# Kernel optimization log

Measured on AMD Instinct MI355X. Metric: run time of the kernel, lower is better.

## Reference

```python
import jax, jax.numpy as jnp
import numpy as np

B, N, INDIM = 512, 200, 200
D1, D2, D3 = 32, 32, 8
RATIO = 0.5
K1 = int(np.ceil(RATIO * N))    # 100 nodes kept after pool1
K2 = int(np.ceil(RATIO * K1))   # 50 nodes kept after pool2
BN_EPS = 1e-5
NEG = -1e9


def setup_inputs() -> dict:
    key = jax.random.key(0)
    ks = jax.random.split(key, 16)
    x = jax.random.normal(ks[0], (B, N, INDIM), jnp.float32)
    u = jax.random.uniform(ks[1], (B, N, N), jnp.float32)
    ut = jnp.triu(jnp.where(u > 0.9, u, 0.0), 1)
    adj = ut + jnp.swapaxes(ut, 1, 2)
    g = lambda i, shape: jax.random.normal(ks[i], shape, jnp.float32) * 0.1
    return dict(
        x=x, adj=adj,
        W1=g(2, (INDIM, D1)), a1s=g(3, (D1,)), a1d=g(4, (D1,)), b1=jnp.zeros((D1,), jnp.float32),
        W2=g(5, (D1, D2)), a2s=g(6, (D2,)), a2d=g(7, (D2,)), b2=jnp.zeros((D2,), jnp.float32),
        pw1=g(8, (D1,)), pw2=g(9, (D2,)),
        fc1_w=g(10, ((D1 + D2) * 2, D2)), fc1_b=jnp.zeros((D2,), jnp.float32),
        fc2_w=g(11, (D2, D3)), fc2_b=jnp.zeros((D3,), jnp.float32),
        fc3_w=g(12, (D3, 2)), fc3_b=jnp.zeros((2,), jnp.float32),
        bn4_g=jnp.ones((D2,), jnp.float32), bn4_b=jnp.zeros((D2,), jnp.float32),
        bn5_g=jnp.ones((D3,), jnp.float32), bn5_b=jnp.zeros((D3,), jnp.float32))


def _gat(x, mask, W, a_s, a_d, b):
    # PyG GATConv (heads=1): alpha_ij = softmax_j LeakyReLU(a_d.h_i + a_s.h_j) over in-neighbors j (self-loops added)
    h = jnp.einsum('bnf,fd->bnd', x, W)
    es = h @ a_s                    # [B,n] source term
    ed = h @ a_d                    # [B,n] dest term
    m = mask | jnp.eye(mask.shape[1], dtype=bool)
    logits = jax.nn.leaky_relu(ed[:, :, None] + es[:, None, :], 0.2)
    alpha = jax.nn.softmax(jnp.where(m, logits, NEG), axis=-1)   # [B,n,n]
    return jnp.einsum('bij,bjd->bid', alpha, h) + b


def _topk(x, adj_w, w, k):
    # TopKPooling(multiplier=1, nonlinearity=sigmoid): score = sigmoid(x.w/||w||)
    score = jax.nn.sigmoid((x @ w) / (jnp.linalg.norm(w) + 1e-16))   # [B,n]
    vals, idx = jax.lax.top_k(score, k)                              # perm sorted desc, as PyG
    xk = jnp.take_along_axis(x, idx[:, :, None], axis=1) * vals[:, :, None]
    ak = jnp.take_along_axis(jnp.take_along_axis(adj_w, idx[:, :, None], axis=1), idx[:, None, :], axis=2)
    return xk, ak, vals


def _bn(z, g, b):
    # eval-mode BatchNorm1d: running_mean=0, running_var=1
    return g * z / jnp.sqrt(1.0 + BN_EPS) + b


def reference(x, adj, W1, a1s, a1d, b1, W2, a2s, a2d, b2, pw1, pw2,
              fc1_w, fc1_b, fc2_w, fc2_b, fc3_w, fc3_b, bn4_g, bn4_b, bn5_g, bn5_b):
    h = _gat(x, adj > 0, W1, a1s, a1d, b1)
    h, aw, s1 = _topk(h, adj, pw1, K1)
    x1 = jnp.concatenate([h.max(axis=1), h.mean(axis=1)], axis=1)    # [B, 64]
    # augment_adj: add self-loops, spspmm (A+I)@(A+I), remove self-loops
    eye = jnp.eye(K1, dtype=aw.dtype)
    a2 = jnp.einsum('bij,bjk->bik', aw + eye, aw + eye) * (1.0 - eye)
    h = _gat(h, a2 != 0, W2, a2s, a2d, b2)
    h, _, s2 = _topk(h, a2, pw2, K2)
    x2 = jnp.concatenate([h.max(axis=1), h.mean(axis=1)], axis=1)    # [B, 64]
    z = jnp.concatenate([x1, x2], axis=1)                            # [B, 128]
    z = _bn(jax.nn.relu(z @ fc1_w + fc1_b), bn4_g, bn4_b)            # dropout: eval -> identity
    z = _bn(jax.nn.relu(z @ fc2_w + fc2_b), bn5_g, bn5_b)
    logp = jax.nn.log_softmax(z @ fc3_w + fc3_b, axis=-1)            # [B, 2]
    return logp, s1, s2
```

## Files before the change

### kernel.cpp

```cpp
#include <hip/hip_runtime.h>
#include <math.h>

#define N_   200
#define B_   512
#define K1_  100
#define K2_  50

#define S1_OFF 1024
#define S2_OFF 52224

__device__ __forceinline__ float lrelu(float v) { return v > 0.f ? v : 0.2f * v; }
__device__ __forceinline__ float sigm(float v)  { return 1.f / (1.f + __expf(-v)); }

__device__ __forceinline__ void bitonic_desc(float* key, int* idx, int n, int t) {
  for (int k = 2; k <= n; k <<= 1) {
    for (int j = k >> 1; j > 0; j >>= 1) {
      __syncthreads();
      int ixj = t ^ j;
      if (t < n && ixj > t) {
        float a = key[t], c = key[ixj];
        int ia = idx[t], ic = idx[ixj];
        bool gt = (a > c) || (a == c && ia < ic);
        if (((t & k) == 0) ? !gt : gt) {
          key[t] = c; key[ixj] = a; idx[t] = ic; idx[ixj] = ia;
        }
      }
    }
  }
  __syncthreads();
}


__global__ __launch_bounds__(256) void gnn_fused(
    const float* __restrict__ x, const float* __restrict__ adj,
    const float* __restrict__ W1, const float* __restrict__ a1s,
    const float* __restrict__ a1d, const float* __restrict__ b1,
    const float* __restrict__ W2g, const float* __restrict__ a2s,
    const float* __restrict__ a2d, const float* __restrict__ b2,
    const float* __restrict__ pw1, const float* __restrict__ pw2,
    const float* __restrict__ fc1w, const float* __restrict__ fc1b,
    const float* __restrict__ fc2w, const float* __restrict__ fc2b,
    const float* __restrict__ fc3w, const float* __restrict__ fc3b,
    const float* __restrict__ bn4g, const float* __restrict__ bn4b,
    const float* __restrict__ bn5g, const float* __restrict__ bn5b,
    float* __restrict__ out)
{
  __shared__ __align__(16) char smem[63792];
  float*    sH    = (float*)smem;
  float*    sH1   = (float*)(smem + 25600);
  float*    sXK   = (float*)(smem + 38400);
  float*    sES   = (float*)(smem + 51200);
  float*    sED   = (float*)(smem + 52000);
  unsigned* sBITS = (unsigned*)(smem + 52800);
  float*    sW2   = (float*)(smem + 52800);
  float*    sKey  = (float*)(smem + 58400);
  int*      sIdx  = (int*)(smem + 59424);
  int*      sSel  = (int*)(smem + 60448);
  float*    sVal  = (float*)(smem + 60848);
  float*    sXV   = (float*)(smem + 61248);
  float*    sRed  = (float*)(smem + 61760);
  unsigned* sMask2= (unsigned*)(smem + 61792);

  const int t = threadIdx.x;
  const int b = blockIdx.x;
  const float* xb = x   + (size_t)b * N_ * N_;
  const float* ab = adj + (size_t)b * N_ * N_;

  if (t < N_) {
    float acc[32];
    #pragma unroll
    for (int d = 0; d < 32; ++d) acc[d] = 0.f;
    const float* xr = xb + t * N_;
    for (int k = 0; k < N_; k += 4) {
      float4 xv = *(const float4*)(xr + k);
      #pragma unroll
      for (int kk = 0; kk < 4; ++kk) {
        float xs = (&xv.x)[kk];
        const float* wr = W1 + (k + kk) * 32;
        #pragma unroll
        for (int d = 0; d < 32; ++d) acc[d] += xs * wr[d];
      }
    }
    float es = 0.f, ed = 0.f;
    #pragma unroll
    for (int d = 0; d < 32; ++d) { es += acc[d] * a1s[d]; ed += acc[d] * a1d[d]; }
    sES[t] = es; sED[t] = ed;
    #pragma unroll
    for (int d = 0; d < 32; ++d) sH[t * 32 + d] = acc[d];
  }
  __syncthreads();

  {
    float v = (t < N_) ? sES[t] : -3.0e38f;
    #pragma unroll
    for (int off = 1; off < 64; off <<= 1) v = fmaxf(v, __shfl_xor(v, off, 64));
    if ((t & 63) == 0) sRed[t >> 6] = v;
  }
  __syncthreads();
  {
    float esmax = fmaxf(fmaxf(sRed[0], sRed[1]), fmaxf(sRed[2], sRed[3]));

    if (t < N_) {
      const float* arow = ab + (size_t)t * N_;
      float ed_i = sED[t];
      float L = lrelu(ed_i + esmax);
      float ssum = 0.f;
      float acc[32];
      #pragma unroll
      for (int d = 0; d < 32; ++d) acc[d] = 0.f;
      for (int jw = 0; jw < 7; ++jw) {
        int jbase = jw * 32;
        int cnt = (jw < 6) ? 32 : 8;
        unsigned mb = 0u;
        for (int j4 = 0; j4 < cnt; j4 += 4) {
          float4 av = *(const float4*)(arow + jbase + j4);
          #pragma unroll
          for (int jj = 0; jj < 4; ++jj) {
            int j = jbase + j4 + jj;
            float a = (&av.x)[jj];
            bool conn = a > 0.f;
            if (conn) mb |= (1u << (j4 + jj));
            float w = 0.f;
            if (conn || j == t) w = __expf(lrelu(ed_i + sES[j]) - L);
            ssum += w;
            const float* hr = &sH[j * 32];
            #pragma unroll
            for (int d = 0; d < 32; ++d) acc[d] += w * hr[d];
          }
        }
        sBITS[t * 7 + jw] = mb;
      }
      float inv = 1.f / ssum;
      #pragma unroll
      for (int d = 0; d < 32; ++d) sH1[t * 32 + d] = acc[d] * inv + b1[d];
    }
  }
  __syncthreads();

  {
    float npw = 0.f;
    #pragma unroll
    for (int d = 0; d < 32; ++d) npw += pw1[d] * pw1[d];
    npw = sqrtf(npw) + 1e-16f;
    float sc = -1.f;
    if (t < N_) {
      float dp = 0.f;
      #pragma unroll
      for (int d = 0; d < 32; ++d) dp += sH1[t * 32 + d] * pw1[d];
      sc = sigm(dp / npw);
    }
    sKey[t] = sc; sIdx[t] = t;
  }
  bitonic_desc(sKey, sIdx, 256, t);
  if (t < K1_) {
    out[S1_OFF + b * K1_ + t] = sKey[t];
    sVal[t] = sKey[t]; sSel[t] = sIdx[t];
  }
  __syncthreads();
  {
    float tmp[13];
    #pragma unroll
    for (int it = 0; it < 13; ++it) {
      int i = t + it * 256;
      if (i < K1_ * 32) tmp[it] = sH1[sSel[i >> 5] * 32 + (i & 31)] * sVal[i >> 5];
    }
    __syncthreads();
    #pragma unroll
    for (int it = 0; it < 13; ++it) {
      int i = t + it * 256;
      if (i < K1_ * 32) sXK[i] = tmp[it];
    }
  }
  __syncthreads();
  if (t < 32) {
    float m = -3.0e38f, s = 0.f;
    for (int r = 0; r < K1_; ++r) { float v = sXK[r * 32 + t]; m = fmaxf(m, v); s += v; }
    sXV[t] = m; sXV[32 + t] = s / 100.f;
  }

  if (t < K1_) {
    int gi = sSel[t];
    #pragma unroll
    for (int w = 0; w < 4; ++w) {
      unsigned m = 0;
      const int lim = (w < 3) ? 32 : 4;
      for (int jj = 0; jj < lim; ++jj) {
        int j = w * 32 + jj;
        int gj = sSel[j];
        unsigned bit = (sBITS[gi * 7 + (gj >> 5)] >> (gj & 31)) & 1u;
        if (j == t) bit = 1u;
        m |= bit << jj;
      }
      sMask2[t * 5 + w] = m;
    }
  }
  __syncthreads();
  {
    unsigned pr0 = 0, pr1 = 0, pr2 = 0, pr3 = 0;
    if (t < K1_) {
      #pragma unroll
      for (int kw = 0; kw < 4; ++kw) {
        unsigned mk = sMask2[t * 5 + kw];
        const int lim = (kw < 3) ? 32 : 4;
        for (int kk = 0; kk < lim; ++kk) {
          if ((mk >> kk) & 1u) {
            int k = kw * 32 + kk;
            pr0 |= sMask2[k * 5 + 0]; pr1 |= sMask2[k * 5 + 1];
            pr2 |= sMask2[k * 5 + 2]; pr3 |= sMask2[k * 5 + 3];
          }
        }
      }
    }
    __syncthreads();
    if (t < K1_) {
      sMask2[t * 5 + 0] = pr0; sMask2[t * 5 + 1] = pr1;
      sMask2[t * 5 + 2] = pr2; sMask2[t * 5 + 3] = pr3;
    }
  }
  __syncthreads();

  for (int i = t; i < 1024; i += 256) sW2[i] = W2g[i];
  __syncthreads();
  if (t < K1_) {
    float acc[32];
    #pragma unroll
    for (int d = 0; d < 32; ++d) acc[d] = 0.f;
    for (int k = 0; k < 32; ++k) {
      float xv = sXK[t * 32 + k];
      const float* wr = &sW2[k * 32];
      #pragma unroll
      for (int d = 0; d < 32; ++d) acc[d] += xv * wr[d];
    }
    float es = 0.f, ed = 0.f;
    #pragma unroll
    for (int d = 0; d < 32; ++d) { es += acc[d] * a2s[d]; ed += acc[d] * a2d[d]; }
    sES[t] = es; sED[t] = ed;
    #pragma unroll
    for (int d = 0; d < 32; ++d) sH[t * 32 + d] = acc[d];
  }
  __syncthreads();
  {
    float v = (t < K1_) ? sES[t] : -3.0e38f;
    #pragma unroll
    for (int off = 1; off < 64; off <<= 1) v = fmaxf(v, __shfl_xor(v, off, 64));
    if ((t & 63) == 0) sRed[t >> 6] = v;
  }
  __syncthreads();
  {
    float esm2 = fmaxf(fmaxf(sRed[0], sRed[1]), fmaxf(sRed[2], sRed[3]));
    if (t < K1_) {
      float ed_i = sED[t];
      float L = lrelu(ed_i + esm2);
      float ssum = 0.f;
      float acc[32];
      #pragma unroll
      for (int d = 0; d < 32; ++d) acc[d] = 0.f;
      #pragma unroll
      for (int jw = 0; jw < 4; ++jw) {
        unsigned mw = sMask2[t * 5 + jw];
        const int lim = (jw < 3) ? 32 : 4;
        for (int jj = 0; jj < lim; ++jj) {
          int j = jw * 32 + jj;
          float w = 0.f;
          if ((mw >> jj) & 1u) w = __expf(lrelu(ed_i + sES[j]) - L);
          ssum += w;
          const float* hr = &sH[j * 32];
          #pragma unroll
          for (int d = 0; d < 32; ++d) acc[d] += w * hr[d];
        }
      }
      float inv = 1.f / ssum;
      #pragma unroll
      for (int d = 0; d < 32; ++d) sH1[t * 32 + d] = acc[d] * inv + b2[d];
    }
  }
  __syncthreads();

  {
    float npw = 0.f;
    #pragma unroll
    for (int d = 0; d < 32; ++d) npw += pw2[d] * pw2[d];
    npw = sqrtf(npw) + 1e-16f;
    float sc = -1.f;
    if (t < K1_) {
      float dp = 0.f;
      #pragma unroll
      for (int d = 0; d < 32; ++d) dp += sH1[t * 32 + d] * pw2[d];
      sc = sigm(dp / npw);
    }
    if (t < 128) { sKey[t] = sc; sIdx[t] = t; }
  }
  bitonic_desc(sKey, sIdx, 128, t);
  if (t < K2_) {
    out[S2_OFF + b * K2_ + t] = sKey[t];
    sVal[t] = sKey[t]; sSel[t] = sIdx[t];
  }
  __syncthreads();
  {
    int d = t & 31, r0 = t >> 5;
    for (int r = r0; r < K2_; r += 8) sXK[r * 32 + d] = sH1[sSel[r] * 32 + d] * sVal[r];
  }
  __syncthreads();
  if (t < 32) {
    float m = -3.0e38f, s = 0.f;
    for (int r = 0; r < K2_; ++r) { float v = sXK[r * 32 + t]; m = fmaxf(m, v); s += v; }
    sXV[64 + t] = m; sXV[96 + t] = s / 50.f;
  }
  __syncthreads();

  const float RS = 0.99999500003749969f;
  if (t < 32) {
    float z = fc1b[t];
    for (int k = 0; k < 128; ++k) z += sXV[k] * fc1w[k * 32 + t];
    z = fmaxf(z, 0.f);
    z = bn4g[t] * z * RS + bn4b[t];
    sKey[t] = z;
  }
  __syncthreads();
  if (t < 8) {
    float z = fc2b[t];
    for (int k = 0; k < 32; ++k) z += sKey[k] * fc2w[k * 8 + t];
    z = fmaxf(z, 0.f);
    z = bn5g[t] * z * RS + bn5b[t];
    sKey[32 + t] = z;
  }
  __syncthreads();
  if (t < 2) {
    float z = fc3b[t];
    for (int k = 0; k < 8; ++k) z += sKey[32 + k] * fc3w[k * 2 + t];
    sKey[40 + t] = z;
  }
  __syncthreads();
  if (t < 2) {
    float z0 = sKey[40], z1 = sKey[41];
    float m = fmaxf(z0, z1);
    float lse = m + logf(__expf(z0 - m) + __expf(z1 - m));
    out[b * 2 + t] = sKey[40 + t] - lse;
  }
}

extern "C" void kernel_launch(void* const* d_in, const int* in_sizes, int n_in,
                              void* d_out, int out_size, void* d_ws, size_t ws_size,
                              hipStream_t stream) {
  (void)in_sizes; (void)n_in; (void)d_ws; (void)ws_size; (void)out_size;
  const float* x    = (const float*)d_in[0];
  const float* adj  = (const float*)d_in[1];
  const float* W1   = (const float*)d_in[2];
  const float* a1s  = (const float*)d_in[3];
  const float* a1d  = (const float*)d_in[4];
  const float* b1   = (const float*)d_in[5];
  const float* W2   = (const float*)d_in[6];
  const float* a2s  = (const float*)d_in[7];
  const float* a2d  = (const float*)d_in[8];
  const float* b2   = (const float*)d_in[9];
  const float* pw1  = (const float*)d_in[10];
  const float* pw2  = (const float*)d_in[11];
  const float* fc1w = (const float*)d_in[12];
  const float* fc1b = (const float*)d_in[13];
  const float* fc2w = (const float*)d_in[14];
  const float* fc2b = (const float*)d_in[15];
  const float* fc3w = (const float*)d_in[16];
  const float* fc3b = (const float*)d_in[17];
  const float* bn4g = (const float*)d_in[18];
  const float* bn4b = (const float*)d_in[19];
  const float* bn5g = (const float*)d_in[20];
  const float* bn5b = (const float*)d_in[21];

  gnn_fused<<<B_, 256, 0, stream>>>(x, adj, W1, a1s, a1d, b1, W2, a2s, a2d, b2,
                                    pw1, pw2, fc1w, fc1b, fc2w, fc2b, fc3w, fc3b,
                                    bn4g, bn4b, bn5g, bn5b, (float*)d_out);
}
```

Baseline: 332.6 us.

## Split feature dimension across 512 threads per block with padded shared rows

Doubles the block to 512 threads and splits the 32-wide feature dimension across thread groups: 2 groups of 16 for GAT1 and 4 groups of 8 for GAT2. Partial attention scalars are reduced through extra shared buffers. Shared rows are padded to a stride of 36 to reduce bank conflicts, and the W2 load is moved earlier to overlap with mask squaring. The aim is more parallelism per graph and lower per-thread register use, at the cost of more shared memory (lower blocks per CU) and duplicated adjacency reads and exp work across the feature groups.

```diff
diff --git a/kernel.cpp b/kernel.cpp
--- a/kernel.cpp
+++ b/kernel.cpp
@@ -5,6 +5,7 @@
 #define B_   512
 #define K1_  100
 #define K2_  50
+#define ST   36
 
 #define S1_OFF 1024
 #define S2_OFF 52224
@@ -31,7 +32,7 @@
 }
 
 
-__global__ __launch_bounds__(256) void gnn_fused(
+__global__ __launch_bounds__(512, 4) void gnn_fused(
     const float* __restrict__ x, const float* __restrict__ adj,
     const float* __restrict__ W1, const float* __restrict__ a1s,
     const float* __restrict__ a1d, const float* __restrict__ b1,
@@ -45,95 +46,109 @@
     const float* __restrict__ bn5g, const float* __restrict__ bn5b,
     float* __restrict__ out)
 {
-  __shared__ __align__(16) char smem[63792];
+  __shared__ __align__(16) char smem[74736];
   float*    sH    = (float*)smem;
-  float*    sH1   = (float*)(smem + 25600);
-  float*    sXK   = (float*)(smem + 38400);
-  float*    sES   = (float*)(smem + 51200);
-  float*    sED   = (float*)(smem + 52000);
-  unsigned* sBITS = (unsigned*)(smem + 52800);
-  float*    sW2   = (float*)(smem + 52800);
-  float*    sKey  = (float*)(smem + 58400);
-  int*      sIdx  = (int*)(smem + 59424);
-  int*      sSel  = (int*)(smem + 60448);
-  float*    sVal  = (float*)(smem + 60848);
-  float*    sXV   = (float*)(smem + 61248);
-  float*    sRed  = (float*)(smem + 61760);
-  unsigned* sMask2= (unsigned*)(smem + 61792);
+  float*    sH1   = (float*)(smem + 28800);
+  float*    sXK   = (float*)(smem + 43200);
+  float*    sES   = (float*)(smem + 57600);
+  float*    sED   = (float*)(smem + 58624);
+  float*    sES2  = (float*)(smem + 59648);
+  float*    sED2  = (float*)(smem + 61696);
+  unsigned* sBITS = (unsigned*)(smem + 63744);
+  float*    sW2   = (float*)(smem + 63744);
+  float*    sKey  = (float*)(smem + 69344);
+  int*      sIdx  = (int*)(smem + 70368);
+  int*      sSel  = (int*)(smem + 71392);
+  float*    sVal  = (float*)(smem + 71792);
+  float*    sXV   = (float*)(smem + 72192);
+  float*    sRed  = (float*)(smem + 72704);
+  unsigned* sMask2= (unsigned*)(smem + 72736);
 
   const int t = threadIdx.x;
   const int b = blockIdx.x;
+  const int n = t & 255;
+  const int d0 = __builtin_amdgcn_readfirstlane((t >> 8) << 4);
   const float* xb = x   + (size_t)b * N_ * N_;
   const float* ab = adj + (size_t)b * N_ * N_;
 
-  if (t < N_) {
-    float acc[32];
-    #pragma unroll
-    for (int d = 0; d < 32; ++d) acc[d] = 0.f;
-    const float* xr = xb + t * N_;
+  if (n < N_) {
+    float acc[16];
+    #pragma unroll
+    for (int d = 0; d < 16; ++d) acc[d] = 0.f;
+    const float* xr = xb + n * N_;
+    const float* Wh = W1 + d0;
     for (int k = 0; k < N_; k += 4) {
       float4 xv = *(const float4*)(xr + k);
       #pragma unroll
       for (int kk = 0; kk < 4; ++kk) {
         float xs = (&xv.x)[kk];
-        const float* wr = W1 + (k + kk) * 32;
+        const float* wr = Wh + (k + kk) * 32;
         #pragma unroll
-        for (int d = 0; d < 32; ++d) acc[d] += xs * wr[d];
+        for (int d = 0; d < 16; ++d) acc[d] += xs * wr[d];
       }
     }
     float es = 0.f, ed = 0.f;
     #pragma unroll
-    for (int d = 0; d < 32; ++d) { es += acc[d] * a1s[d]; ed += acc[d] * a1d[d]; }
-    sES[t] = es; sED[t] = ed;
-    #pragma unroll
-    for (int d = 0; d < 32; ++d) sH[t * 32 + d] = acc[d];
-  }
-  __syncthreads();
-
-  {
-    float v = (t < N_) ? sES[t] : -3.0e38f;
+    for (int d = 0; d < 16; ++d) { es += acc[d] * a1s[d0 + d]; ed += acc[d] * a1d[d0 + d]; }
+    sES2[t] = es; sED2[t] = ed;
+    #pragma unroll
+    for (int d = 0; d < 16; ++d) sH[n * ST + d0 + d] = acc[d];
+  }
+  __syncthreads();
+
+  float esmax;
+  {
+    float v = -3.0e38f;
+    if (t < N_) {
+      float es = sES2[t] + sES2[t + 256];
+      float ed = sED2[t] + sED2[t + 256];
+      sES[t] = es; sED[t] = ed; v = es;
+    }
     #pragma unroll
     for (int off = 1; off < 64; off <<= 1) v = fmaxf(v, __shfl_xor(v, off, 64));
     if ((t & 63) == 0) sRed[t >> 6] = v;
   }
   __syncthreads();
   {
-    float esmax = fmaxf(fmaxf(sRed[0], sRed[1]), fmaxf(sRed[2], sRed[3]));
-
-    if (t < N_) {
-      const float* arow = ab + (size_t)t * N_;
-      float ed_i = sED[t];
-      float L = lrelu(ed_i + esmax);
-      float ssum = 0.f;
-      float acc[32];
-      #pragma unroll
-      for (int d = 0; d < 32; ++d) acc[d] = 0.f;
-      for (int jw = 0; jw < 7; ++jw) {
-        int jbase = jw * 32;
-        int cnt = (jw < 6) ? 32 : 8;
-        unsigned mb = 0u;
-        for (int j4 = 0; j4 < cnt; j4 += 4) {
-          float4 av = *(const float4*)(arow + jbase + j4);
+    float m = sRed[0];
+    #pragma unroll
+    for (int i = 1; i < 8; ++i) m = fmaxf(m, sRed[i]);
+    esmax = m;
+  }
+
+  if (n < N_) {
+    const float* arow = ab + (size_t)n * N_;
+    float ed_i = sED[n];
+    float L = lrelu(ed_i + esmax);
+    float ssum = 0.f;
+    float acc[16];
+    #pragma unroll
+    for (int d = 0; d < 16; ++d) acc[d] = 0.f;
+    for (int jw = 0; jw < 7; ++jw) {
+      int jbase = jw * 32;
+      int cnt = (jw < 6) ? 32 : 8;
+      unsigned mb = 0u;
+      for (int j4 = 0; j4 < cnt; j4 += 4) {
+        float4 av = *(const float4*)(arow + jbase + j4);
+        #pragma unroll
+        for (int jj = 0; jj < 4; ++jj) {
+          int j = jbase + j4 + jj;
+          float a = (&av.x)[jj];
+          bool conn = a > 0.f;
+          if (conn) mb |= (1u << (j4 + jj));
+          float w = 0.f;
+          if (conn || j == n) w = __expf(lrelu(ed_i + sES[j]) - L);
+          ssum += w;
+          const float* hr = &sH[j * ST + d0];
           #pragma unroll
-          for (int jj = 0; jj < 4; ++jj) {
-            int j = jbase + j4 + jj;
-            float a = (&av.x)[jj];
-            bool conn = a > 0.f;
-            if (conn) mb |= (1u << (j4 + jj));
-            float w = 0.f;
-            if (conn || j == t) w = __expf(lrelu(ed_i + sES[j]) - L);
-            ssum += w;
-            const float* hr = &sH[j * 32];
-            #pragma unroll
-            for (int d = 0; d < 32; ++d) acc[d] += w * hr[d];
-          }
+          for (int d = 0; d < 16; ++d) acc[d] += w * hr[d];
         }
-        sBITS[t * 7 + jw] = mb;
-      }
-      float inv = 1.f / ssum;
-      #pragma unroll
-      for (int d = 0; d < 32; ++d) sH1[t * 32 + d] = acc[d] * inv + b1[d];
-    }
+      }
+      if (d0 == 0) sBITS[n * 7 + jw] = mb;
+    }
+    float inv = 1.f / ssum;
+    #pragma unroll
+    for (int d = 0; d < 16; ++d) sH1[n * ST + d0 + d] = acc[d] * inv + b1[d0 + d];
   }
   __syncthreads();
 
@@ -146,10 +161,10 @@
     if (t < N_) {
       float dp = 0.f;
       #pragma unroll
-      for (int d = 0; d < 32; ++d) dp += sH1[t * 32 + d] * pw1[d];
+      for (int d = 0; d < 32; ++d) dp += sH1[t * ST + d] * pw1[d];
       sc = sigm(dp / npw);
     }
-    sKey[t] = sc; sIdx[t] = t;
+    if (t < 256) { sKey[t] = sc; sIdx[t] = t; }
   }
   bitonic_desc(sKey, sIdx, 256, t);
   if (t < K1_) {
@@ -158,23 +173,23 @@
   }
   __syncthreads();
   {
-    float tmp[13];
-    #pragma unroll
-    for (int it = 0; it < 13; ++it) {
-      int i = t + it * 256;
-      if (i < K1_ * 32) tmp[it] = sH1[sSel[i >> 5] * 32 + (i & 31)] * sVal[i >> 5];
+    float tmp[7];
+    #pragma unroll
+    for (int it = 0; it < 7; ++it) {
+      int i = t + it * 512;
+      if (i < K1_ * 32) tmp[it] = sH1[sSel[i >> 5] * ST + (i & 31)] * sVal[i >> 5];
     }
     __syncthreads();
     #pragma unroll
-    for (int it = 0; it < 13; ++it) {
-      int i = t + it * 256;
-      if (i < K1_ * 32) sXK[i] = tmp[it];
+    for (int it = 0; it < 7; ++it) {
+      int i = t + it * 512;
+      if (i < K1_ * 32) sXK[(i >> 5) * ST + (i & 31)] = tmp[it];
     }
   }
   __syncthreads();
   if (t < 32) {
     float m = -3.0e38f, s = 0.f;
-    for (int r = 0; r < K1_; ++r) { float v = sXK[r * 32 + t]; m = fmaxf(m, v); s += v; }
+    for (int r = 0; r < K1_; ++r) { float v = sXK[r * ST + t]; m = fmaxf(m, v); s += v; }
     sXV[t] = m; sXV[32 + t] = s / 100.f;
   }
 
@@ -195,6 +210,7 @@
     }
   }
   __syncthreads();
+  for (int i = t; i < 1024; i += 512) sW2[i] = W2g[i];
   {
     unsigned pr0 = 0, pr1 = 0, pr2 = 0, pr3 = 0;
     if (t < K1_) {
@@ -219,60 +235,74 @@
   }
   __syncthreads();
 
-  for (int i = t; i < 1024; i += 256) sW2[i] = W2g[i];
-  __syncthreads();
-  if (t < K1_) {
-    float acc[32];
-    #pragma unroll
-    for (int d = 0; d < 32; ++d) acc[d] = 0.f;
+  const int qE  = __builtin_amdgcn_readfirstlane(t >> 7);
+  const int d0e = qE << 3;
+  const int nE  = t & 127;
+  if (nE < K1_) {
+    float xk[32];
+    #pragma unroll
+    for (int k = 0; k < 32; k += 4) *(float4*)&xk[k] = *(const float4*)&sXK[nE * ST + k];
+    float acc[8];
+    #pragma unroll
+    for (int d = 0; d < 8; ++d) acc[d] = 0.f;
+    #pragma unroll
     for (int k = 0; k < 32; ++k) {
-      float xv = sXK[t * 32 + k];
-      const float* wr = &sW2[k * 32];
+      float xv = xk[k];
+      const float* wr = &sW2[k * 32 + d0e];
       #pragma unroll
-      for (int d = 0; d < 32; ++d) acc[d] += xv * wr[d];
+      for (int d = 0; d < 8; ++d) acc[d] += xv * wr[d];
     }
     float es = 0.f, ed = 0.f;
     #pragma unroll
-    for (int d = 0; d < 32; ++d) { es += acc[d] * a2s[d]; ed += acc[d] * a2d[d]; }
-    sES[t] = es; sED[t] = ed;
-    #pragma unroll
-    for (int d = 0; d < 32; ++d) sH[t * 32 + d] = acc[d];
-  }
-  __syncthreads();
-  {
-    float v = (t < K1_) ? sES[t] : -3.0e38f;
+    for (int d = 0; d < 8; ++d) { es += acc[d] * a2s[d0e + d]; ed += acc[d] * a2d[d0e + d]; }
+    sES2[t] = es; sED2[t] = ed;
+    #pragma unroll
+    for (int d = 0; d < 8; ++d) sH[nE * ST + d0e + d] = acc[d];
+  }
+  __syncthreads();
+  float esm2;
+  {
+    float v = -3.0e38f;
+    if (t < K1_) {
+      float es = sES2[t] + sES2[t + 128] + sES2[t + 256] + sES2[t + 384];
+      float ed = sED2[t] + sED2[t + 128] + sED2[t + 256] + sED2[t + 384];
+      sES[t] = es; sED[t] = ed; v = es;
+    }
     #pragma unroll
     for (int off = 1; off < 64; off <<= 1) v = fmaxf(v, __shfl_xor(v, off, 64));
     if ((t & 63) == 0) sRed[t >> 6] = v;
   }
   __syncthreads();
   {
-    float esm2 = fmaxf(fmaxf(sRed[0], sRed[1]), fmaxf(sRed[2], sRed[3]));
-    if (t < K1_) {
-      float ed_i = sED[t];
-      float L = lrelu(ed_i + esm2);
-      float ssum = 0.f;
-      float acc[32];
-      #pragma unroll
-      for (int d = 0; d < 32; ++d) acc[d] = 0.f;
-      #pragma unroll
-      for (int jw = 0; jw < 4; ++jw) {
-        unsigned mw = sMask2[t * 5 + jw];
-        const int lim = (jw < 3) ? 32 : 4;
-        for (int jj = 0; jj < lim; ++jj) {
-          int j = jw * 32 + jj;
-          float w = 0.f;
-          if ((mw >> jj) & 1u) w = __expf(lrelu(ed_i + sES[j]) - L);
-          ssum += w;
-          const float* hr = &sH[j * 32];
-          #pragma unroll
-          for (int d = 0; d < 32; ++d) acc[d] += w * hr[d];
-        }
-      }
-      float inv = 1.f / ssum;
-      #pragma unroll
-      for (int d = 0; d < 32; ++d) sH1[t * 32 + d] = acc[d] * inv + b2[d];
-    }
+    float m = sRed[0];
+    #pragma unroll
+    for (int i = 1; i < 8; ++i) m = fmaxf(m, sRed[i]);
+    esm2 = m;
+  }
+  if (nE < K1_) {
+    float ed_i = sED[nE];
+    float L = lrelu(ed_i + esm2);
+    float ssum = 0.f;
+    float acc[8];
+    #pragma unroll
+    for (int d = 0; d < 8; ++d) acc[d] = 0.f;
+    #pragma unroll
+    for (int jw = 0; jw < 4; ++jw) {
+      unsigned mw = sMask2[nE * 5 + jw];
+      const int lim = (jw < 3) ? 32 : 4;
+      for (int jj = 0; jj < lim; ++jj) {
+        int j = jw * 32 + jj;
+        float w = 0.f;
+        if ((mw >> jj) & 1u) w = __expf(lrelu(ed_i + sES[j]) - L);
+        ssum += w;
+        const float* hr = &sH[j * ST + d0e];
+        #pragma unroll
+        for (int d = 0; d < 8; ++d) acc[d] += w * hr[d];
+      }
+    }
+    float inv = 1.f / ssum;
+    #pragma unroll
+    for (int d = 0; d < 8; ++d) sH1[nE * ST + d0e + d] = acc[d] * inv + b2[d0e + d];
   }
   __syncthreads();
 
@@ -285,7 +315,7 @@
     if (t < K1_) {
       float dp = 0.f;
       #pragma unroll
-      for (int d = 0; d < 32; ++d) dp += sH1[t * 32 + d] * pw2[d];
+      for (int d = 0; d < 32; ++d) dp += sH1[t * ST + d] * pw2[d];
       sc = sigm(dp / npw);
     }
     if (t < 128) { sKey[t] = sc; sIdx[t] = t; }
@@ -297,13 +327,16 @@
   }
   __syncthreads();
   {
-    int d = t & 31, r0 = t >> 5;
-    for (int r = r0; r < K2_; r += 8) sXK[r * 32 + d] = sH1[sSel[r] * 32 + d] * sVal[r];
+    #pragma unroll
+    for (int it = 0; it < 4; ++it) {
+      int i = t + it * 512;
+      if (i < K2_ * 32) sXK[(i >> 5) * ST + (i & 31)] = sH1[sSel[i >> 5] * ST + (i & 31)] * sVal[i >> 5];
+    }
   }
   __syncthreads();
   if (t < 32) {
     float m = -3.0e38f, s = 0.f;
-    for (int r = 0; r < K2_; ++r) { float v = sXK[r * 32 + t]; m = fmaxf(m, v); s += v; }
+    for (int r = 0; r < K2_; ++r) { float v = sXK[r * ST + t]; m = fmaxf(m, v); s += v; }
     sXV[64 + t] = m; sXV[96 + t] = s / 50.f;
   }
   __syncthreads();
@@ -366,7 +399,7 @@
   const float* bn5g = (const float*)d_in[20];
   const float* bn5b = (const float*)d_in[21];
 
-  gnn_fused<<<B_, 256, 0, stream>>>(x, adj, W1, a1s, a1d, b1, W2, a2s, a2d, b2,
+  gnn_fused<<<B_, 512, 0, stream>>>(x, adj, W1, a1s, a1d, b1, W2, a2s, a2d, b2,
                                     pw1, pw2, fc1w, fc1b, fc2w, fc2b, fc3w, fc3b,
                                     bn4g, bn4b, bn5g, bn5b, (float*)d_out);
 }
```

Result: slower. 861.2 us (+158.9%).
